# Kernel optimization log

Measured on AMD Instinct MI355X. Metric: run time of the kernel, lower is better.

## Reference

```python
import jax, jax.numpy as jnp
import numpy as np

DIM = 256      # model width (l1 projects scalar -> DIM)
P = 256        # S5 state dimension
BATCH, L = 8, 4096


def setup_inputs() -> dict:
    key = jax.random.key(0)
    ks = jax.random.split(key, 16)
    d, p = DIM, P
    inp = {}
    inp['x'] = jax.random.normal(ks[0], (BATCH, L, 1), jnp.float32)
    # l1: Linear(1, dim)
    inp['l1_w'] = jax.random.normal(ks[1], (d, 1), jnp.float32)
    inp['l1_b'] = jnp.zeros((d,), jnp.float32)
    # S5 diagonal SSM parameters (complex split into re/im)
    inp['lam_re'] = -(0.5 + 0.5 * jax.random.uniform(ks[2], (p,), jnp.float32))
    inp['lam_im'] = jnp.pi * jnp.arange(p, dtype=jnp.float32)
    inp['B_re'] = jax.random.normal(ks[3], (p, d), jnp.float32) / np.sqrt(d)
    inp['B_im'] = jax.random.normal(ks[4], (p, d), jnp.float32) / np.sqrt(d)
    inp['C_re'] = jax.random.normal(ks[5], (d, p), jnp.float32) / np.sqrt(p)
    inp['C_im'] = jax.random.normal(ks[6], (d, p), jnp.float32) / np.sqrt(p)
    inp['D'] = jax.random.normal(ks[7], (d,), jnp.float32)
    log_lo, log_hi = np.log(1e-3), np.log(1e-1)
    inp['log_step'] = log_lo + (log_hi - log_lo) * jax.random.uniform(ks[8], (p,), jnp.float32)
    # ff_enc: Linear(dim, dim*10); ff_dec: Linear(dim*10, dim)
    inp['ff_enc_w'] = jax.random.normal(ks[9], (10 * d, d), jnp.float32) / np.sqrt(d)
    inp['ff_enc_b'] = jnp.zeros((10 * d,), jnp.float32)
    inp['ff_dec_w'] = jax.random.normal(ks[10], (d, 10 * d), jnp.float32) / np.sqrt(10 * d)
    inp['ff_dec_b'] = jnp.zeros((d,), jnp.float32)
    # l2: Linear(dim, 1)
    inp['l2_w'] = jax.random.normal(ks[11], (1, d), jnp.float32) / np.sqrt(d)
    inp['l2_b'] = jnp.zeros((1,), jnp.float32)
    return inp


def _s5_scan(u, lam_re, lam_im, B_re, B_im, C_re, C_im, D, log_step):
    """Diagonal S5 layer: ZOH discretization + parallel associative scan.
    u: [B, L, H] real. Returns [B, L, H] real."""
    lam = (lam_re + 1j * lam_im).astype(jnp.complex64)          # [P]
    step = jnp.exp(log_step).astype(jnp.complex64)               # [P]
    lam_bar = jnp.exp(lam * step)                                # [P]
    Bm = (B_re + 1j * B_im).astype(jnp.complex64)                # [P, H]
    B_bar = ((lam_bar - 1.0) / lam)[:, None] * Bm                # [P, H] (ZOH)
    Bu = jnp.einsum('blh,ph->blp', u.astype(jnp.complex64), B_bar)   # [B, L, P]
    A = jnp.broadcast_to(lam_bar, Bu.shape)

    def binop(e1, e2):
        a1, b1 = e1
        a2, b2 = e2
        return a1 * a2, a2 * b1 + b2

    _, xs = jax.lax.associative_scan(binop, (A, Bu), axis=1)     # [B, L, P]
    Cm = (C_re + 1j * C_im).astype(jnp.complex64)                # [H, P]
    # conj-symmetric parameterization -> 2 * Re(C x) + D * u
    return 2.0 * jnp.einsum('blp,hp->blh', xs, Cm).real + D * u


def reference(x, l1_w, l1_b, lam_re, lam_im, B_re, B_im, C_re, C_im, D,
              log_step, ff_enc_w, ff_enc_b, ff_dec_w, ff_dec_b, l2_w, l2_b):
    # l1: scalar -> dim
    h = x @ l1_w.T + l1_b                                        # [B, L, DIM]
    res = h
    s = _s5_scan(h, lam_re, lam_im, B_re, B_im, C_re, C_im, D, log_step)
    h = jnp.tanh(s) + res                                        # tanh residual
    # dropout layers are identity in eval mode
    res = h
    f = jnp.tanh(h @ ff_enc_w.T + ff_enc_b)                      # [B, L, 10*DIM]
    h = f @ ff_dec_w.T + ff_dec_b + res                          # [B, L, DIM]
    out = h @ l2_w.T + l2_b                                      # [B, L, 1]
    return out
```

## Files before the change

kernel.cpp:

```cpp
#include <hip/hip_runtime.h>

#define DIMD 256
#define PDIM 256
#define NB   8
#define LSEQ 4096
#define MTOT (NB*LSEQ)
#define FDIM 2560
#define NCHUNK 64
#define CLEN 64

typedef __attribute__((ext_vector_type(8))) short s8bf;
typedef __attribute__((ext_vector_type(4))) float f32x4;

#define MFMA16(a,b,c) __builtin_amdgcn_mfma_f32_16x16x32_bf16((a),(b),(c),0,0,0)

static const size_t OFF_LBR  = 0;
static const size_t OFF_LBI  = 256;
static const size_t OFF_A64R = 512;
static const size_t OFF_A64I = 768;
static const size_t OFF_WR   = 1024;
static const size_t OFF_WI   = 1280;
static const size_t OFF_CR   = 1536;
static const size_t OFF_CI   = 1792;
static const size_t OFF_DBL2 = 2048;
static const size_t OFF_E_RE   = 4096;
static const size_t OFF_E_IM   = OFF_E_RE   + 131072;
static const size_t OFF_CAR_RE = OFF_E_IM   + 131072;
static const size_t OFF_CAR_IM = OFF_CAR_RE + 131072;
static const size_t OFF_H1     = OFF_CAR_IM + 131072;
static const size_t OFF_ENC16  = OFF_H1     + 4194304;
static const size_t OFF_DL     = OFF_ENC16  + 327680;
static const size_t OFF_CC16   = OFF_DL     + 327680;

__device__ __forceinline__ ushort f2bf(float f) {
    union { float f; unsigned u; } v; v.f = f;
    unsigned u = v.u;
    return (ushort)((u + 0x7FFFu + ((u >> 16) & 1u)) >> 16);
}
__device__ __forceinline__ float bf2f(ushort h) {
    union { unsigned u; float f; } v; v.u = ((unsigned)h) << 16;
    return v.f;
}
__device__ __forceinline__ float fast_tanh(float x) {
    float e = __expf(2.f * x);
    return 1.f - 2.f * __builtin_amdgcn_rcpf(e + 1.f);
}

__global__ void k_prep(const float* __restrict__ enc_w, const float* __restrict__ dec_w,
                       const float* __restrict__ C_re, const float* __restrict__ C_im,
                       const float* __restrict__ l1w, const float* __restrict__ l1b,
                       const float* __restrict__ lam_re, const float* __restrict__ lam_im,
                       const float* __restrict__ B_re, const float* __restrict__ B_im,
                       const float* __restrict__ log_step, const float* __restrict__ dec_b,
                       const float* __restrict__ l2w, const float* __restrict__ l2b,
                       ushort* __restrict__ enc16, ushort* __restrict__ cc16,
                       float* __restrict__ dlv, float* __restrict__ ws) {
    __shared__ float red[4];
    int bid = blockIdx.x, t = threadIdx.x;
    if (bid < 2560) {
        int i = bid * 256 + t;
        enc16[i] = f2bf(enc_w[i]);
    } else if (bid < 3072) {
        int j = (bid - 2560) * 256 + t;
        int h = j >> 9, c = j & 511;
        int p = c >> 1;
        float v = ((c & 1) == 0) ? 2.f * C_re[h * 256 + p] : -2.f * C_im[h * 256 + p];
        cc16[j] = f2bf(v);
    } else if (bid == 3072) {
        int p = t;
        float st = expf(log_step[p]);
        float lr = lam_re[p], li = lam_im[p];
        float zr = lr * st, zi = li * st;
        float er = expf(zr);
        float lbr = er * cosf(zi), lbi = er * sinf(zi);
        float den = lr * lr + li * li;
        float nr = lbr - 1.0f, ni = lbi;
        float facr = (nr * lr + ni * li) / den;
        float faci = (ni * lr - nr * li) / den;
        float dwr = 0.f, dwi = 0.f, dbr = 0.f, dbi = 0.f;
        for (int h = 0; h < DIMD; ++h) {
            float br = B_re[p * DIMD + h], bi = B_im[p * DIMD + h];
            float w1 = l1w[h], b1 = l1b[h];
            dwr = fmaf(br, w1, dwr); dwi = fmaf(bi, w1, dwi);
            dbr = fmaf(br, b1, dbr); dbi = fmaf(bi, b1, dbi);
        }
        float wr = facr * dwr - faci * dwi, wi = facr * dwi + faci * dwr;
        float cr = facr * dbr - faci * dbi, ci = facr * dbi + faci * dbr;
        float ar = lbr, ai = lbi;
        for (int s = 0; s < 6; ++s) { float tq = ar * ar - ai * ai; ai = 2.f * ar * ai; ar = tq; }
        ws[OFF_LBR + p] = lbr;  ws[OFF_LBI + p] = lbi;
        ws[OFF_A64R + p] = ar;  ws[OFF_A64I + p] = ai;
        ws[OFF_WR + p] = wr;    ws[OFF_WI + p] = wi;
        ws[OFF_CR + p] = cr;    ws[OFF_CI + p] = ci;
        float s = dec_b[t] * l2w[t];
        #pragma unroll
        for (int off = 1; off < 64; off <<= 1) s += __shfl_xor(s, off, 64);
        if ((t & 63) == 0) red[t >> 6] = s;
        __syncthreads();
        if (t == 0) ws[OFF_DBL2] = red[0] + red[1] + red[2] + red[3] + l2b[0];
    } else {
        int k = (bid - 3073) * 256 + t;
        float s0 = 0.f, s1 = 0.f;
        for (int n = 0; n < 256; n += 2) {
            s0 = fmaf(dec_w[(size_t)n * FDIM + k], l2w[n], s0);
            s1 = fmaf(dec_w[(size_t)(n + 1) * FDIM + k], l2w[n + 1], s1);
        }
        dlv[k] = s0 + s1;
    }
}

__global__ void k_scanA(const float* __restrict__ x, float* __restrict__ ws) {
    int p = threadIdx.x, chunk = blockIdx.x, b = blockIdx.y;
    float lbr = ws[OFF_LBR + p], lbi = ws[OFF_LBI + p];
    float wr = ws[OFF_WR + p], wi = ws[OFF_WI + p];
    float cr = ws[OFF_CR + p], ci = ws[OFF_CI + p];
    const float* xb = x + (size_t)b * LSEQ + chunk * CLEN;
    float sr = 0.f, si = 0.f;
    for (int t = 0; t < CLEN; ++t) {
        float xv = xb[t];
        float bur = fmaf(xv, wr, cr), bui = fmaf(xv, wi, ci);
        float nsr = fmaf(lbr, sr, fmaf(-lbi, si, bur));
        float nsi = fmaf(lbr, si, fmaf(lbi, sr, bui));
        sr = nsr; si = nsi;
    }
    size_t idx = ((size_t)b * NCHUNK + chunk) * PDIM + p;
    ws[OFF_E_RE + idx] = sr; ws[OFF_E_IM + idx] = si;
}

__global__ void k_scanB(float* __restrict__ ws) {
    int p = threadIdx.x, b = blockIdx.x;
    float ar = ws[OFF_A64R + p], ai = ws[OFF_A64I + p];
    float sr = 0.f, si = 0.f;
    for (int c = 0; c < NCHUNK; ++c) {
        size_t idx = ((size_t)b * NCHUNK + c) * PDIM + p;
        ws[OFF_CAR_RE + idx] = sr; ws[OFF_CAR_IM + idx] = si;
        float er = ws[OFF_E_RE + idx], ei = ws[OFF_E_IM + idx];
        float nsr = fmaf(ar, sr, fmaf(-ai, si, er));
        float nsi = fmaf(ar, si, fmaf(ai, sr, ei));
        sr = nsr; si = nsi;
    }
}

__global__ __launch_bounds__(256) void k_scg(
        const float* __restrict__ x, const float* __restrict__ ws,
        const ushort* __restrict__ cc16, const float* __restrict__ l1w,
        const float* __restrict__ l1b, const float* __restrict__ Dv,
        ushort* __restrict__ h1) {
    __shared__ ushort xs[64 * 512];
    __shared__ float xbuf[64];
    const int t = threadIdx.x;
    const int chunk = blockIdx.x, b = blockIdx.y;
    const size_t row0 = (size_t)b * LSEQ + chunk * CLEN;
    if (t < 64) xbuf[t] = x[row0 + t];
    const int p = t;
    float lbr = ws[OFF_LBR + p], lbi = ws[OFF_LBI + p];
    float wr = ws[OFF_WR + p], wi = ws[OFF_WI + p];
    float cr = ws[OFF_CR + p], ci = ws[OFF_CI + p];
    size_t cidx = ((size_t)b * NCHUNK + chunk) * PDIM + p;
    float sr = ws[OFF_CAR_RE + cidx], si = ws[OFF_CAR_IM + cidx];
    __syncthreads();
    for (int tt = 0; tt < CLEN; ++tt) {
        float xv = xbuf[tt];
        float bur = fmaf(xv, wr, cr), bui = fmaf(xv, wi, ci);
        float nsr = fmaf(lbr, sr, fmaf(-lbi, si, bur));
        float nsi = fmaf(lbr, si, fmaf(lbi, sr, bui));
        sr = nsr; si = nsi;
        unsigned pk;
        asm("v_cvt_pk_bf16_f32 %0, %1, %2" : "=v"(pk) : "v"(sr), "v"(si));
        *(unsigned*)((char*)xs + tt * 1024 + ((p * 4) ^ ((tt & 7) << 4))) = pk;
    }
    __syncthreads();
    const int w = t >> 6, l = t & 63, lr = l & 15, lg = l >> 4;
    const f32x4 fz = {0.f, 0.f, 0.f, 0.f};
    f32x4 acc[4][4];
    #pragma unroll
    for (int mi = 0; mi < 4; ++mi)
        #pragma unroll
        for (int nj = 0; nj < 4; ++nj) acc[mi][nj] = fz;
    for (int ks = 0; ks < 16; ++ks) {
        s8bf a[4];
        #pragma unroll
        for (int mi = 0; mi < 4; ++mi) {
            int row = mi * 16 + lr;
            a[mi] = *(const s8bf*)((const char*)xs + row * 1024 + ((ks * 64 + lg * 16) ^ ((row & 7) << 4)));
        }
        #pragma unroll
        for (int nj = 0; nj < 4; ++nj) {
            int n = w * 64 + nj * 16 + lr;
            s8bf bfrag = *(const s8bf*)(cc16 + (size_t)n * 512 + ks * 32 + lg * 8);
            #pragma unroll
            for (int mi = 0; mi < 4; ++mi)
                acc[mi][nj] = MFMA16(a[mi], bfrag, acc[mi][nj]);
        }
    }
    #pragma unroll
    for (int nj = 0; nj < 4; ++nj) {
        int n = w * 64 + nj * 16 + lr;
        float l1wn = l1w[n], l1bn = l1b[n], dn = Dv[n];
        #pragma unroll
        for (int mi = 0; mi < 4; ++mi)
            #pragma unroll
            for (int r = 0; r < 4; ++r) {
                int mrow = mi * 16 + lg * 4 + r;
                float u = fmaf(xbuf[mrow], l1wn, l1bn);
                float s = fmaf(dn, u, acc[mi][nj][r]);
                h1[(row0 + mrow) * DIMD + n] = f2bf(fast_tanh(s) + u);
            }
    }
}

__global__ __launch_bounds__(512, 2) void k_ff3(
        const ushort* __restrict__ h1g, const ushort* __restrict__ enc16,
        const float* __restrict__ enc_b, const float* __restrict__ dlv,
        const float* __restrict__ l2w, const float* __restrict__ wsc,
        float* __restrict__ out) {
    __shared__ ushort h1s[64 * 256];
    __shared__ float osum[64];
    const int t = threadIdx.x;
    const int m0 = blockIdx.x * 64;
    const int w = t >> 6, l = t & 63;
    const int lr = l & 15, lg = l >> 4;

    #pragma unroll
    for (int e = 0; e < 4; ++e) {
        int flat = e * 512 + t;
        int row = flat >> 5, unit = flat & 31;
        s8bf v = *(const s8bf*)(h1g + (size_t)(m0 + row) * 256 + unit * 8);
        *(s8bf*)((char*)h1s + row * 512 + ((unit * 16) ^ ((row & 7) << 4))) = v;
    }
    __syncthreads();

    {
        const int m = t >> 3, j = t & 7;
        float rs = 0.f;
        #pragma unroll
        for (int q = 0; q < 4; ++q) {
            int n = j * 32 + q * 8;
            s8bf v = *(const s8bf*)((const char*)h1s + m * 512 + ((2 * n) ^ ((m & 7) << 4)));
            #pragma unroll
            for (int e = 0; e < 8; ++e)
                rs = fmaf(bf2f((ushort)v[e]), l2w[n + e], rs);
        }
        rs += __shfl_xor(rs, 1, 8);
        rs += __shfl_xor(rs, 2, 8);
        rs += __shfl_xor(rs, 4, 8);
        if (j == 0) osum[m] = rs + wsc[OFF_DBL2];
    }

    s8bf aReg[4][8];
    #pragma unroll
    for (int mi = 0; mi < 4; ++mi) {
        int row = mi * 16 + lr;
        #pragma unroll
        for (int kd = 0; kd < 8; ++kd) {
            int kb = kd * 64 + lg * 16;
            aReg[mi][kd] = *(const s8bf*)((const char*)h1s + row * 512 + (kb ^ ((row & 7) << 4)));
        }
    }
    __syncthreads();

    const f32x4 fz = {0.f, 0.f, 0.f, 0.f};
    float dacc[4][4] = {{0.f}};
    const ushort* encBase = enc16 + (size_t)(w * 16 + lr) * 256;

    for (int c = 0; c < 20; ++c) {
        const int k0 = c * 128;
        const int kc = k0 + w * 16 + lr;
        f32x4 facc[4] = {fz, fz, fz, fz};
        const ushort* encRow = encBase + (size_t)k0 * 256;
        #pragma unroll
        for (int kd = 0; kd < 8; ++kd) {
            s8bf bfrag = *(const s8bf*)(encRow + kd * 32 + lg * 8);
            #pragma unroll
            for (int mi = 0; mi < 4; ++mi)
                facc[mi] = MFMA16(aReg[mi][kd], bfrag, facc[mi]);
        }
        float ebv = enc_b[kc];
        float dlk = dlv[kc];
        #pragma unroll
        for (int mi = 0; mi < 4; ++mi)
            #pragma unroll
            for (int r = 0; r < 4; ++r)
                dacc[mi][r] = fmaf(fast_tanh(facc[mi][r] + ebv), dlk, dacc[mi][r]);
    }
    #pragma unroll
    for (int mi = 0; mi < 4; ++mi)
        #pragma unroll
        for (int r = 0; r < 4; ++r) {
            float s = dacc[mi][r];
            s += __shfl_xor(s, 1, 16);
            s += __shfl_xor(s, 2, 16);
            s += __shfl_xor(s, 4, 16);
            s += __shfl_xor(s, 8, 16);
            if (lr == 0) atomicAdd(&osum[mi * 16 + 4 * lg + r], s);
        }
    __syncthreads();
    if (t < 64) out[m0 + t] = osum[t];
}

extern "C" void kernel_launch(void* const* d_in, const int* in_sizes, int n_in,
                              void* d_out, int out_size, void* d_ws, size_t ws_size,
                              hipStream_t stream) {
    const float* x       = (const float*)d_in[0];
    const float* l1w     = (const float*)d_in[1];
    const float* l1b     = (const float*)d_in[2];
    const float* lam_re  = (const float*)d_in[3];
    const float* lam_im  = (const float*)d_in[4];
    const float* B_re    = (const float*)d_in[5];
    const float* B_im    = (const float*)d_in[6];
    const float* C_re    = (const float*)d_in[7];
    const float* C_im    = (const float*)d_in[8];
    const float* Dv      = (const float*)d_in[9];
    const float* log_stp = (const float*)d_in[10];
    const float* enc_w   = (const float*)d_in[11];
    const float* enc_b   = (const float*)d_in[12];
    const float* dec_w   = (const float*)d_in[13];
    const float* dec_b   = (const float*)d_in[14];
    const float* l2w     = (const float*)d_in[15];
    const float* l2b     = (const float*)d_in[16];
    float* ws  = (float*)d_ws;
    float* out = (float*)d_out;
    ushort* h1_16 = (ushort*)(ws + OFF_H1);
    ushort* enc16 = (ushort*)(ws + OFF_ENC16);
    float*  dlv   = ws + OFF_DL;
    ushort* cc16  = (ushort*)(ws + OFF_CC16);

    hipLaunchKernelGGL(k_prep, dim3(3083), dim3(256), 0, stream,
                       enc_w, dec_w, C_re, C_im, l1w, l1b, lam_re, lam_im,
                       B_re, B_im, log_stp, dec_b, l2w, l2b,
                       enc16, cc16, dlv, ws);
    hipLaunchKernelGGL(k_scanA, dim3(NCHUNK, NB), dim3(256), 0, stream, x, ws);
    hipLaunchKernelGGL(k_scanB, dim3(NB), dim3(256), 0, stream, ws);
    hipLaunchKernelGGL(k_scg, dim3(NCHUNK, NB), dim3(256), 0, stream,
                       x, ws, cc16, l1w, l1b, Dv, h1_16);
    hipLaunchKernelGGL(k_ff3, dim3(MTOT / 64), dim3(512), 0, stream,
                       h1_16, enc16, enc_b, dlv, l2w, ws, out);
}
```

Before: 232.7 us.

## Retile fused FFN kernel to 32-row blocks with wider per-wave column tiles

Replaces the 512-thread, 64-row FFN kernel with a 256-thread, 32-row version. Each wave now covers 64 hidden columns per chunk, over 10 chunks, instead of 16 columns over 20 chunks. A fragments are re-read from LDS on every k-step rather than held in registers, which frees registers and should allow more resident blocks. The cost is that each weight fragment now serves only 2 row tiles instead of 4, and the grid is twice as large, so the encoder weights are read from L2 twice as many times in total.

```diff
diff --git a/kernel.cpp b/kernel.cpp
--- a/kernel.cpp
+++ b/kernel.cpp
@@ -209,21 +209,21 @@
     }
 }
 
-__global__ __launch_bounds__(512, 2) void k_ff3(
+__global__ __launch_bounds__(256) void k_ff6(
         const ushort* __restrict__ h1g, const ushort* __restrict__ enc16,
         const float* __restrict__ enc_b, const float* __restrict__ dlv,
         const float* __restrict__ l2w, const float* __restrict__ wsc,
         float* __restrict__ out) {
-    __shared__ ushort h1s[64 * 256];
-    __shared__ float osum[64];
+    __shared__ ushort h1s[32 * 256];
+    __shared__ float osum[32];
     const int t = threadIdx.x;
-    const int m0 = blockIdx.x * 64;
+    const int m0 = blockIdx.x * 32;
     const int w = t >> 6, l = t & 63;
     const int lr = l & 15, lg = l >> 4;
 
     #pragma unroll
     for (int e = 0; e < 4; ++e) {
-        int flat = e * 512 + t;
+        int flat = e * 256 + t;
         int row = flat >> 5, unit = flat & 31;
         s8bf v = *(const s8bf*)(h1g + (size_t)(m0 + row) * 256 + unit * 8);
         *(s8bf*)((char*)h1s + row * 512 + ((unit * 16) ^ ((row & 7) << 4))) = v;
@@ -246,45 +246,47 @@
         rs += __shfl_xor(rs, 4, 8);
         if (j == 0) osum[m] = rs + wsc[OFF_DBL2];
     }
-
-    s8bf aReg[4][8];
+    __syncthreads();
+
+    const f32x4 fz = {0.f, 0.f, 0.f, 0.f};
+    float dacc[2][4] = {{0.f}};
+    const ushort* encBase = enc16 + (size_t)(w * 64 + lr) * 256;
+
+    for (int c = 0; c < 10; ++c) {
+        const int k0 = c * 256;
+        const size_t cOff = (size_t)k0 * 256;
+        f32x4 facc[2][4];
+        #pragma unroll
+        for (int mi = 0; mi < 2; ++mi)
+            #pragma unroll
+            for (int g = 0; g < 4; ++g) facc[mi][g] = fz;
+        #pragma unroll
+        for (int kd = 0; kd < 8; ++kd) {
+            const int kb = kd * 64 + lg * 16;
+            s8bf a0 = *(const s8bf*)((const char*)h1s + lr * 512 + (kb ^ ((lr & 7) << 4)));
+            int row1 = 16 + lr;
+            s8bf a1 = *(const s8bf*)((const char*)h1s + row1 * 512 + (kb ^ ((row1 & 7) << 4)));
+            #pragma unroll
+            for (int g = 0; g < 4; ++g) {
+                s8bf bfrag = *(const s8bf*)(encBase + cOff + (size_t)g * 16 * 256 + kd * 32 + lg * 8);
+                facc[0][g] = MFMA16(a0, bfrag, facc[0][g]);
+                facc[1][g] = MFMA16(a1, bfrag, facc[1][g]);
+            }
+        }
+        #pragma unroll
+        for (int g = 0; g < 4; ++g) {
+            const int kc = k0 + w * 64 + g * 16 + lr;
+            float ebv = enc_b[kc];
+            float dlk = dlv[kc];
+            #pragma unroll
+            for (int mi = 0; mi < 2; ++mi)
+                #pragma unroll
+                for (int r = 0; r < 4; ++r)
+                    dacc[mi][r] = fmaf(fast_tanh(facc[mi][g][r] + ebv), dlk, dacc[mi][r]);
+        }
+    }
     #pragma unroll
-    for (int mi = 0; mi < 4; ++mi) {
-        int row = mi * 16 + lr;
-        #pragma unroll
-        for (int kd = 0; kd < 8; ++kd) {
-            int kb = kd * 64 + lg * 16;
-            aReg[mi][kd] = *(const s8bf*)((const char*)h1s + row * 512 + (kb ^ ((row & 7) << 4)));
-        }
-    }
-    __syncthreads();
-
-    const f32x4 fz = {0.f, 0.f, 0.f, 0.f};
-    float dacc[4][4] = {{0.f}};
-    const ushort* encBase = enc16 + (size_t)(w * 16 + lr) * 256;
-
-    for (int c = 0; c < 20; ++c) {
-        const int k0 = c * 128;
-        const int kc = k0 + w * 16 + lr;
-        f32x4 facc[4] = {fz, fz, fz, fz};
-        const ushort* encRow = encBase + (size_t)k0 * 256;
-        #pragma unroll
-        for (int kd = 0; kd < 8; ++kd) {
-            s8bf bfrag = *(const s8bf*)(encRow + kd * 32 + lg * 8);
-            #pragma unroll
-            for (int mi = 0; mi < 4; ++mi)
-                facc[mi] = MFMA16(aReg[mi][kd], bfrag, facc[mi]);
-        }
-        float ebv = enc_b[kc];
-        float dlk = dlv[kc];
-        #pragma unroll
-        for (int mi = 0; mi < 4; ++mi)
-            #pragma unroll
-            for (int r = 0; r < 4; ++r)
-                dacc[mi][r] = fmaf(fast_tanh(facc[mi][r] + ebv), dlk, dacc[mi][r]);
-    }
-    #pragma unroll
-    for (int mi = 0; mi < 4; ++mi)
+    for (int mi = 0; mi < 2; ++mi)
         #pragma unroll
         for (int r = 0; r < 4; ++r) {
             float s = dacc[mi][r];
@@ -295,7 +297,7 @@
             if (lr == 0) atomicAdd(&osum[mi * 16 + 4 * lg + r], s);
         }
     __syncthreads();
-    if (t < 64) out[m0 + t] = osum[t];
+    if (t < 32) out[m0 + t] = osum[t];
 }
 
 extern "C" void kernel_launch(void* const* d_in, const int* in_sizes, int n_in,
@@ -333,6 +335,6 @@
     hipLaunchKernelGGL(k_scanB, dim3(NB), dim3(256), 0, stream, ws);
     hipLaunchKernelGGL(k_scg, dim3(NCHUNK, NB), dim3(256), 0, stream,
                        x, ws, cc16, l1w, l1b, Dv, h1_16);
-    hipLaunchKernelGGL(k_ff3, dim3(MTOT / 64), dim3(512), 0, stream,
+    hipLaunchKernelGGL(k_ff6, dim3(MTOT / 32), dim3(256), 0, stream,
                        h1_16, enc16, enc_b, dlv, l2w, ws, out);
 }
```

Measured after the change: 300.7 us. +29.2%, slower.

## Fuse carry scan, S5 output and FF block into one kernel with fragment-ordered weights

Applied to the files above, without the earlier changes.

Removes the separate carry-propagation kernel: each chunk block recomputes its incoming state by serially combining the preceding chunk end-states. Fuses the S5 output GEMM with the feed-forward/l2 stage, so h1 stays in shared memory and never makes a global round trip. Reorders the bf16 encoder and C weights in the prep kernel into MFMA fragment order so that B loads are contiguous. In exchange, the fused kernel runs with 256 threads over 512 blocks instead of 512-thread blocks, the carry recompute is redundant serial work growing with the chunk index, and register pressure rises with the 4x4 facc tile.

```diff
diff --git a/kernel.cpp b/kernel.cpp
--- a/kernel.cpp
+++ b/kernel.cpp
@@ -25,12 +25,9 @@
 static const size_t OFF_DBL2 = 2048;
 static const size_t OFF_E_RE   = 4096;
 static const size_t OFF_E_IM   = OFF_E_RE   + 131072;
-static const size_t OFF_CAR_RE = OFF_E_IM   + 131072;
-static const size_t OFF_CAR_IM = OFF_CAR_RE + 131072;
-static const size_t OFF_H1     = OFF_CAR_IM + 131072;
-static const size_t OFF_ENC16  = OFF_H1     + 4194304;
-static const size_t OFF_DL     = OFF_ENC16  + 327680;
-static const size_t OFF_CC16   = OFF_DL     + 327680;
+static const size_t OFF_ENC16F = OFF_E_IM   + 131072;
+static const size_t OFF_DL     = OFF_ENC16F + 327680;
+static const size_t OFF_CC16F  = OFF_DL     + 2560;
 
 __device__ __forceinline__ ushort f2bf(float f) {
     union { float f; unsigned u; } v; v.f = f;
@@ -53,19 +50,22 @@
                        const float* __restrict__ B_re, const float* __restrict__ B_im,
                        const float* __restrict__ log_step, const float* __restrict__ dec_b,
                        const float* __restrict__ l2w, const float* __restrict__ l2b,
-                       ushort* __restrict__ enc16, ushort* __restrict__ cc16,
+                       ushort* __restrict__ enc16f, ushort* __restrict__ cc16f,
                        float* __restrict__ dlv, float* __restrict__ ws) {
     __shared__ float red[4];
     int bid = blockIdx.x, t = threadIdx.x;
     if (bid < 2560) {
-        int i = bid * 256 + t;
-        enc16[i] = f2bf(enc_w[i]);
+        int j = bid * 256 + t;
+        int e = j & 7, lr = (j >> 3) & 15, lg = (j >> 7) & 3, kd = (j >> 9) & 7, ft = j >> 12;
+        enc16f[j] = f2bf(enc_w[(size_t)(ft * 16 + lr) * 256 + kd * 32 + lg * 8 + e]);
     } else if (bid < 3072) {
         int j = (bid - 2560) * 256 + t;
-        int h = j >> 9, c = j & 511;
+        int e = j & 7, lr = (j >> 3) & 15, lg = (j >> 7) & 3, ks = (j >> 9) & 15, nt = j >> 13;
+        int h = nt * 16 + lr;
+        int c = ks * 32 + lg * 8 + e;
         int p = c >> 1;
         float v = ((c & 1) == 0) ? 2.f * C_re[h * 256 + p] : -2.f * C_im[h * 256 + p];
-        cc16[j] = f2bf(v);
+        cc16f[j] = f2bf(v);
     } else if (bid == 3072) {
         int p = t;
         float st = expf(log_step[p]);
@@ -127,37 +127,33 @@
     ws[OFF_E_RE + idx] = sr; ws[OFF_E_IM + idx] = si;
 }
 
-__global__ void k_scanB(float* __restrict__ ws) {
-    int p = threadIdx.x, b = blockIdx.x;
-    float ar = ws[OFF_A64R + p], ai = ws[OFF_A64I + p];
-    float sr = 0.f, si = 0.f;
-    for (int c = 0; c < NCHUNK; ++c) {
-        size_t idx = ((size_t)b * NCHUNK + c) * PDIM + p;
-        ws[OFF_CAR_RE + idx] = sr; ws[OFF_CAR_IM + idx] = si;
-        float er = ws[OFF_E_RE + idx], ei = ws[OFF_E_IM + idx];
-        float nsr = fmaf(ar, sr, fmaf(-ai, si, er));
-        float nsi = fmaf(ar, si, fmaf(ai, sr, ei));
-        sr = nsr; si = nsi;
-    }
-}
-
-__global__ __launch_bounds__(256) void k_scg(
+__global__ __launch_bounds__(256) void k_scf(
         const float* __restrict__ x, const float* __restrict__ ws,
-        const ushort* __restrict__ cc16, const float* __restrict__ l1w,
-        const float* __restrict__ l1b, const float* __restrict__ Dv,
-        ushort* __restrict__ h1) {
+        const ushort* __restrict__ cc16f, const ushort* __restrict__ enc16f,
+        const float* __restrict__ l1w, const float* __restrict__ l1b,
+        const float* __restrict__ Dv, const float* __restrict__ enc_b,
+        const float* __restrict__ dlv, const float* __restrict__ l2w,
+        float* __restrict__ out) {
     __shared__ ushort xs[64 * 512];
     __shared__ float xbuf[64];
+    __shared__ float osum[64];
     const int t = threadIdx.x;
     const int chunk = blockIdx.x, b = blockIdx.y;
     const size_t row0 = (size_t)b * LSEQ + chunk * CLEN;
     if (t < 64) xbuf[t] = x[row0 + t];
     const int p = t;
+    float a64r = ws[OFF_A64R + p], a64i = ws[OFF_A64I + p];
+    float sr = 0.f, si = 0.f;
+    for (int c = 0; c < chunk; ++c) {
+        size_t idx = ((size_t)b * NCHUNK + c) * PDIM + p;
+        float er = ws[OFF_E_RE + idx], ei = ws[OFF_E_IM + idx];
+        float nsr = fmaf(a64r, sr, fmaf(-a64i, si, er));
+        float nsi = fmaf(a64r, si, fmaf(a64i, sr, ei));
+        sr = nsr; si = nsi;
+    }
     float lbr = ws[OFF_LBR + p], lbi = ws[OFF_LBI + p];
     float wr = ws[OFF_WR + p], wi = ws[OFF_WI + p];
     float cr = ws[OFF_CR + p], ci = ws[OFF_CI + p];
-    size_t cidx = ((size_t)b * NCHUNK + chunk) * PDIM + p;
-    float sr = ws[OFF_CAR_RE + cidx], si = ws[OFF_CAR_IM + cidx];
     __syncthreads();
     for (int tt = 0; tt < CLEN; ++tt) {
         float xv = xbuf[tt];
@@ -186,13 +182,15 @@
         }
         #pragma unroll
         for (int nj = 0; nj < 4; ++nj) {
-            int n = w * 64 + nj * 16 + lr;
-            s8bf bfrag = *(const s8bf*)(cc16 + (size_t)n * 512 + ks * 32 + lg * 8);
+            int nt = w * 4 + nj;
+            s8bf bfrag = *(const s8bf*)(cc16f + ((size_t)((nt * 16 + ks) * 4 + lg) * 16 + lr) * 8);
             #pragma unroll
             for (int mi = 0; mi < 4; ++mi)
                 acc[mi][nj] = MFMA16(a[mi], bfrag, acc[mi][nj]);
         }
     }
+    __syncthreads();
+    char* h1s = (char*)xs;
     #pragma unroll
     for (int nj = 0; nj < 4; ++nj) {
         int n = w * 64 + nj * 16 + lr;
@@ -204,84 +202,61 @@
                 int mrow = mi * 16 + lg * 4 + r;
                 float u = fmaf(xbuf[mrow], l1wn, l1bn);
                 float s = fmaf(dn, u, acc[mi][nj][r]);
-                h1[(row0 + mrow) * DIMD + n] = f2bf(fast_tanh(s) + u);
+                *(ushort*)(h1s + mrow * 512 + ((2 * n) ^ ((mrow & 7) << 4))) = f2bf(fast_tanh(s) + u);
             }
     }
-}
-
-__global__ __launch_bounds__(512, 2) void k_ff3(
-        const ushort* __restrict__ h1g, const ushort* __restrict__ enc16,
-        const float* __restrict__ enc_b, const float* __restrict__ dlv,
-        const float* __restrict__ l2w, const float* __restrict__ wsc,
-        float* __restrict__ out) {
-    __shared__ ushort h1s[64 * 256];
-    __shared__ float osum[64];
-    const int t = threadIdx.x;
-    const int m0 = blockIdx.x * 64;
-    const int w = t >> 6, l = t & 63;
-    const int lr = l & 15, lg = l >> 4;
-
-    #pragma unroll
-    for (int e = 0; e < 4; ++e) {
-        int flat = e * 512 + t;
-        int row = flat >> 5, unit = flat & 31;
-        s8bf v = *(const s8bf*)(h1g + (size_t)(m0 + row) * 256 + unit * 8);
-        *(s8bf*)((char*)h1s + row * 512 + ((unit * 16) ^ ((row & 7) << 4))) = v;
-    }
-    __syncthreads();
-
+    __syncthreads();
     {
-        const int m = t >> 3, j = t & 7;
+        const int m = t >> 2, j = t & 3;
         float rs = 0.f;
         #pragma unroll
-        for (int q = 0; q < 4; ++q) {
-            int n = j * 32 + q * 8;
-            s8bf v = *(const s8bf*)((const char*)h1s + m * 512 + ((2 * n) ^ ((m & 7) << 4)));
+        for (int q = 0; q < 8; ++q) {
+            int n = j * 64 + q * 8;
+            s8bf v = *(const s8bf*)(h1s + m * 512 + ((2 * n) ^ ((m & 7) << 4)));
             #pragma unroll
             for (int e = 0; e < 8; ++e)
                 rs = fmaf(bf2f((ushort)v[e]), l2w[n + e], rs);
         }
-        rs += __shfl_xor(rs, 1, 8);
-        rs += __shfl_xor(rs, 2, 8);
-        rs += __shfl_xor(rs, 4, 8);
-        if (j == 0) osum[m] = rs + wsc[OFF_DBL2];
-    }
-
-    s8bf aReg[4][8];
-    #pragma unroll
-    for (int mi = 0; mi < 4; ++mi) {
-        int row = mi * 16 + lr;
+        rs += __shfl_xor(rs, 1, 4);
+        rs += __shfl_xor(rs, 2, 4);
+        if (j == 0) osum[m] = rs + ws[OFF_DBL2];
+    }
+    __syncthreads();
+    float dacc[4][4] = {{0.f}};
+    for (int c = 0; c < 10; ++c) {
+        f32x4 facc[4][4];
+        #pragma unroll
+        for (int g = 0; g < 4; ++g)
+            #pragma unroll
+            for (int mi = 0; mi < 4; ++mi) facc[g][mi] = fz;
         #pragma unroll
         for (int kd = 0; kd < 8; ++kd) {
-            int kb = kd * 64 + lg * 16;
-            aReg[mi][kd] = *(const s8bf*)((const char*)h1s + row * 512 + (kb ^ ((row & 7) << 4)));
-        }
-    }
-    __syncthreads();
-
-    const f32x4 fz = {0.f, 0.f, 0.f, 0.f};
-    float dacc[4][4] = {{0.f}};
-    const ushort* encBase = enc16 + (size_t)(w * 16 + lr) * 256;
-
-    for (int c = 0; c < 20; ++c) {
-        const int k0 = c * 128;
-        const int kc = k0 + w * 16 + lr;
-        f32x4 facc[4] = {fz, fz, fz, fz};
-        const ushort* encRow = encBase + (size_t)k0 * 256;
-        #pragma unroll
-        for (int kd = 0; kd < 8; ++kd) {
-            s8bf bfrag = *(const s8bf*)(encRow + kd * 32 + lg * 8);
+            s8bf a[4];
+            #pragma unroll
+            for (int mi = 0; mi < 4; ++mi) {
+                int row = mi * 16 + lr;
+                a[mi] = *(const s8bf*)(h1s + row * 512 + ((kd * 64 + lg * 16) ^ ((row & 7) << 4)));
+            }
+            #pragma unroll
+            for (int g = 0; g < 4; ++g) {
+                int ft = c * 16 + w * 4 + g;
+                s8bf bfrag = *(const s8bf*)(enc16f + ((size_t)((ft * 8 + kd) * 4 + lg) * 16 + lr) * 8);
+                #pragma unroll
+                for (int mi = 0; mi < 4; ++mi)
+                    facc[g][mi] = MFMA16(a[mi], bfrag, facc[g][mi]);
+            }
+        }
+        #pragma unroll
+        for (int g = 0; g < 4; ++g) {
+            int kc = c * 256 + w * 64 + g * 16 + lr;
+            float ebv = enc_b[kc];
+            float dlk = dlv[kc];
             #pragma unroll
             for (int mi = 0; mi < 4; ++mi)
-                facc[mi] = MFMA16(aReg[mi][kd], bfrag, facc[mi]);
-        }
-        float ebv = enc_b[kc];
-        float dlk = dlv[kc];
-        #pragma unroll
-        for (int mi = 0; mi < 4; ++mi)
-            #pragma unroll
-            for (int r = 0; r < 4; ++r)
-                dacc[mi][r] = fmaf(fast_tanh(facc[mi][r] + ebv), dlk, dacc[mi][r]);
+                #pragma unroll
+                for (int r = 0; r < 4; ++r)
+                    dacc[mi][r] = fmaf(fast_tanh(facc[g][mi][r] + ebv), dlk, dacc[mi][r]);
+        }
     }
     #pragma unroll
     for (int mi = 0; mi < 4; ++mi)
@@ -295,7 +270,7 @@
             if (lr == 0) atomicAdd(&osum[mi * 16 + 4 * lg + r], s);
         }
     __syncthreads();
-    if (t < 64) out[m0 + t] = osum[t];
+    if (t < 64) out[row0 + t] = osum[t];
 }
 
 extern "C" void kernel_launch(void* const* d_in, const int* in_sizes, int n_in,
@@ -320,19 +295,15 @@
     const float* l2b     = (const float*)d_in[16];
     float* ws  = (float*)d_ws;
     float* out = (float*)d_out;
-    ushort* h1_16 = (ushort*)(ws + OFF_H1);
-    ushort* enc16 = (ushort*)(ws + OFF_ENC16);
-    float*  dlv   = ws + OFF_DL;
-    ushort* cc16  = (ushort*)(ws + OFF_CC16);
+    ushort* enc16f = (ushort*)(ws + OFF_ENC16F);
+    float*  dlv    = ws + OFF_DL;
+    ushort* cc16f  = (ushort*)(ws + OFF_CC16F);
 
     hipLaunchKernelGGL(k_prep, dim3(3083), dim3(256), 0, stream,
                        enc_w, dec_w, C_re, C_im, l1w, l1b, lam_re, lam_im,
                        B_re, B_im, log_stp, dec_b, l2w, l2b,
-                       enc16, cc16, dlv, ws);
+                       enc16f, cc16f, dlv, ws);
     hipLaunchKernelGGL(k_scanA, dim3(NCHUNK, NB), dim3(256), 0, stream, x, ws);
-    hipLaunchKernelGGL(k_scanB, dim3(NB), dim3(256), 0, stream, ws);
-    hipLaunchKernelGGL(k_scg, dim3(NCHUNK, NB), dim3(256), 0, stream,
-                       x, ws, cc16, l1w, l1b, Dv, h1_16);
-    hipLaunchKernelGGL(k_ff3, dim3(MTOT / 64), dim3(512), 0, stream,
-                       h1_16, enc16, enc_b, dlv, l2w, ws, out);
-}
+    hipLaunchKernelGGL(k_scf, dim3(NCHUNK, NB), dim3(256), 0, stream,
+                       x, ws, cc16f, enc16f, l1w, l1b, Dv, enc_b, dlv, l2w, out);
+}
```

After: 295.6 us. 27.1% more time.
